# Optimization experiments

Hardware: AMD Instinct MI355X
Metric: run time of the kernel (lower is better)

The kernel has to match this reference:

```python
import jax, jax.numpy as jnp
import numpy as np

B, T, FD, NH, NC, NOUT = 32, 512, 256, 1024, 512, 8


def setup_inputs() -> dict:
    key = jax.random.key(0)
    ks = jax.random.split(key, 12)
    s = lambda k, sh, sc=0.05: (jax.random.normal(k, sh, jnp.float32) * sc)
    return dict(
        x=jax.random.normal(ks[0], (B, T, FD), jnp.float32),
        lens=jax.random.randint(ks[1], (B,), T // 2, T + 1, jnp.int32),
        W1=s(ks[2], (NH, FD)), b1=jnp.zeros((NH,), jnp.float32),
        g1=jnp.ones((NH,), jnp.float32), be1=jnp.zeros((NH,), jnp.float32),
        W2=s(ks[3], (NH, NH)), b2=jnp.zeros((NH,), jnp.float32),
        g2=jnp.ones((NH,), jnp.float32), be2=jnp.zeros((NH,), jnp.float32),
        lstm_wih=s(ks[4], (2, 2, 4 * NC, NH)),   # [layer, dir, 4H, in]
        lstm_whh=s(ks[5], (2, 2, 4 * NC, NC)),   # [layer, dir, 4H, H]
        lstm_bih=s(ks[6], (2, 2, 4 * NC)),
        lstm_bhh=s(ks[7], (2, 2, 4 * NC)),
        w_u=s(ks[8], (2 * NC,)), b_u=jnp.zeros((), jnp.float32),
        Wc=s(ks[9], (NOUT, 2 * NC)), bc=jnp.zeros((NOUT,), jnp.float32),
    )


def _layernorm(x, g, b, eps=1e-5):
    m = x.mean(-1, keepdims=True)
    v = ((x - m) ** 2).mean(-1, keepdims=True)
    return (x - m) / jnp.sqrt(v + eps) * g + b


def _lrelu(z):
    return jnp.where(z >= 0, z, 0.01 * z)  # LeakyReLU default slope


def _lstm_dir(x, wih, whh, bih, bhh):
    # x: [B,T,in] -> h: [B,T,H]; torch gate order i,f,g,o
    Bz = x.shape[0]
    H = whh.shape[1]
    xp = jnp.einsum('bti,gi->btg', x, wih) + bih + bhh  # [B,T,4H]

    def step(carry, xt):
        h, c = carry
        gates = xt + h @ whh.T
        i, f, g, o = jnp.split(gates, 4, axis=-1)
        c = jax.nn.sigmoid(f) * c + jax.nn.sigmoid(i) * jnp.tanh(g)
        h = jax.nn.sigmoid(o) * jnp.tanh(c)
        return (h, c), h

    h0 = jnp.zeros((Bz, H), x.dtype)
    _, hs = jax.lax.scan(step, (h0, h0), xp.transpose(1, 0, 2))
    return hs.transpose(1, 0, 2)


def _bilstm(x, wih, whh, bih, bhh):
    # params indexed [dir, ...]; backward dir processes the full padded
    # sequence reversed (original feeds unpacked pad_sequence to nn.LSTM)
    hf = _lstm_dir(x, wih[0], whh[0], bih[0], bhh[0])
    hb = _lstm_dir(x[:, ::-1], wih[1], whh[1], bih[1], bhh[1])[:, ::-1]
    return jnp.concatenate([hf, hb], axis=-1)


def reference(x, lens, W1, b1, g1, be1, W2, b2, g2, be2,
              lstm_wih, lstm_whh, lstm_bih, lstm_bhh, w_u, b_u, Wc, bc):
    Tn = x.shape[1]
    # extract MLP (dropout = identity in eval)
    h = _lrelu(_layernorm(x @ W1.T + b1, g1, be1))
    h = _lrelu(_layernorm(h @ W2.T + b2, g2, be2))
    # pad_sequence zero-pads AFTER extract -> zero out pad positions
    mask = jnp.arange(Tn)[None, :] < lens[:, None]  # [B,T]
    h = h * mask[..., None]
    # 2-layer bidirectional LSTM over the full padded sequence
    h = _bilstm(h, lstm_wih[0], lstm_whh[0], lstm_bih[0], lstm_bhh[0])
    h = _bilstm(h, lstm_wih[1], lstm_whh[1], lstm_bih[1], lstm_bhh[1])
    # Attn with window_len=1: per-step linear score, masked softmax, weighted sum
    scores = h @ w_u + b_u                          # [B,T]
    scores = jnp.where(mask, scores, -jnp.inf)
    alpha = jax.nn.softmax(scores, axis=-1)
    pooled = jnp.einsum('bt,btd->bd', alpha, h)     # [B, 2*NC]
    return pooled @ Wc.T + bc
```

## Files before the change

kernel.cpp:

```cpp
#include <hip/hip_runtime.h>
#include <stdint.h>
#include <stddef.h>


typedef short  short8  __attribute__((ext_vector_type(8)));
typedef short  short4v __attribute__((ext_vector_type(4)));
typedef float  float4v __attribute__((ext_vector_type(4)));
typedef unsigned long long u64;

__device__ inline float b2f(short x){
  union { unsigned u; float f; } v; v.u = ((unsigned)(unsigned short)x) << 16; return v.f;
}
__device__ inline short f2b(float f){
  union { float f; unsigned u; } v; v.f = f;
  unsigned r = (v.u + 0x7fffu + ((v.u >> 16) & 1u)) >> 16;
  return (short)r;
}
__device__ inline float sigm(float x){ return 1.f / (1.f + __expf(-x)); }
__device__ inline float tanh_(float x){ return 2.f / (1.f + __expf(-2.f*x)) - 1.f; }

__global__ __launch_bounds__(256) void detect_f32(
    const unsigned short* __restrict__ p, unsigned* __restrict__ flag)
{
  const int tid = threadIdx.x;
  unsigned h = 0;
  for (int i = tid; i < 1024; i += 256){
    const unsigned e = (p[i] >> 7) & 0xFFu;
    if (e >= 0xC0u) ++h;
  }
#pragma unroll
  for (int off=32; off>0; off>>=1) h += __shfl_xor(h, off, 64);
  __shared__ unsigned sh[4];
  if ((tid&63)==0) sh[tid>>6] = h;
  __syncthreads();
  if (tid==0) *flag = (sh[0]+sh[1]+sh[2]+sh[3] >= 8u) ? 1u : 0u;
}

__global__ __launch_bounds__(256) void to_bf16(
    const void* __restrict__ src, short* __restrict__ dst, int n,
    const unsigned* __restrict__ flag)
{
  const int i = blockIdx.x*256 + threadIdx.x;
  if (i >= n) return;
  if (*flag) dst[i] = f2b(((const float*)src)[i]);
  else       dst[i] = ((const short*)src)[i];
}

__global__ __launch_bounds__(256) void to_bf16_perm(
    const void* __restrict__ src, short* __restrict__ dst, const int W,
    const int n, const unsigned* __restrict__ flag)
{
  const int i = blockIdx.x*256 + threadIdx.x;
  if (i >= n) return;
  const int col = i % W;
  const int r   = (i / W) % 2048;
  const int blk = i / (W * 2048);
  const int gate = r >> 9, unit = r & 511;
  const size_t j = ((size_t)blk*2048 + (size_t)(unit*4 + gate))*W + col;
  short out = (*flag) ? f2b(((const float*)src)[i]) : ((const short*)src)[i];
  dst[j] = out;
}

__global__ __launch_bounds__(256) void gemm_bt(
    const short* __restrict__ A, const short* __restrict__ W,
    short* __restrict__ C, const short* __restrict__ bias1,
    const short* __restrict__ bias2, int N, int K)
{
  __shared__ __align__(16) short lA[128*40];
  __shared__ __align__(16) short lW[128*40];
  const int tid  = threadIdx.x;
  const int lane = tid & 63, wv = tid >> 6;
  const int wm = wv >> 1, wn = wv & 1;
  const int quad = lane >> 4, l15 = lane & 15;
  const long m0 = (long)blockIdx.y * 128, n0 = (long)blockIdx.x * 128;

  float4v acc[4][4];
#pragma unroll
  for (int i=0;i<4;++i)
#pragma unroll
    for (int j=0;j<4;++j) acc[i][j] = (float4v)0.f;

  const int r  = tid >> 2;
  const int kc = tid & 3;
  const int nkt = K >> 5;
  for (int kt = 0; kt < nkt; ++kt) {
    __syncthreads();
    const short* ga = A + (m0 + r) * (long)K + kt*32 + kc*8;
    const short* gw = W + (n0 + r) * (long)K + kt*32 + kc*8;
    short8 a0 = *(const short8*)ga;
    short8 a1 = *(const short8*)(ga + 64*(long)K);
    short8 w0 = *(const short8*)gw;
    short8 w1 = *(const short8*)(gw + 64*(long)K);
    *(short8*)&lA[r*40 + kc*8]        = a0;
    *(short8*)&lA[(r+64)*40 + kc*8]   = a1;
    *(short8*)&lW[r*40 + kc*8]        = w0;
    *(short8*)&lW[(r+64)*40 + kc*8]   = w1;
    __syncthreads();
    short8 af[4], bfr[4];
#pragma unroll
    for (int i=0;i<4;++i) af[i]  = *(const short8*)&lA[(wm*64 + i*16 + l15)*40 + quad*8];
#pragma unroll
    for (int j=0;j<4;++j) bfr[j] = *(const short8*)&lW[(wn*64 + j*16 + l15)*40 + quad*8];
#pragma unroll
    for (int i=0;i<4;++i)
#pragma unroll
      for (int j=0;j<4;++j)
        acc[i][j] = __builtin_amdgcn_mfma_f32_16x16x32_bf16(af[i], bfr[j], acc[i][j], 0, 0, 0);
  }
#pragma unroll
  for (int j=0;j<4;++j){
    const long n = n0 + wn*64 + j*16 + l15;
    float bs = b2f(bias1[n]);
    if (bias2) bs += b2f(bias2[n]);
#pragma unroll
    for (int i=0;i<4;++i){
      const long mb = m0 + wm*64 + i*16 + quad*4;
#pragma unroll
      for (int g=0; g<4; ++g)
        C[(mb+g)*(long)N + n] = f2b(acc[i][j][g] + bs);
    }
  }
}

__global__ __launch_bounds__(256) void ln_lrelu(
    const short* __restrict__ X, const short* __restrict__ g,
    const short* __restrict__ be, short* __restrict__ out,
    const int* __restrict__ lens, const int domask)
{
  const int row = blockIdx.x, tid = threadIdx.x;
  const short* xr = X + (size_t)row * 1024;
  short4v xv = *(const short4v*)(xr + tid*4);
  float v[4];
#pragma unroll
  for (int k=0;k<4;++k) v[k] = b2f(xv[k]);
  float s  = v[0]+v[1]+v[2]+v[3];
  float sq = v[0]*v[0]+v[1]*v[1]+v[2]*v[2]+v[3]*v[3];
#pragma unroll
  for (int off=32; off>0; off>>=1){
    s  += __shfl_xor(s,  off, 64);
    sq += __shfl_xor(sq, off, 64);
  }
  __shared__ float red[8];
  if ((tid&63)==0){ red[tid>>6] = s; red[4+(tid>>6)] = sq; }
  __syncthreads();
  s  = red[0]+red[1]+red[2]+red[3];
  sq = red[4]+red[5]+red[6]+red[7];
  const float mean = s * (1.f/1024.f);
  const float var  = sq * (1.f/1024.f) - mean*mean;
  const float rstd = rsqrtf(var + 1e-5f);
  float zmul = 1.f;
  if (domask){ const int b = row >> 9, t = row & 511; if (t >= lens[b]) zmul = 0.f; }
  short4v o;
#pragma unroll
  for (int k=0;k<4;++k){
    const int n = tid*4 + k;
    float y = (v[k]-mean)*rstd*b2f(g[n]) + b2f(be[n]);
    y = (y >= 0.f) ? y : 0.01f*y;
    o[k] = f2b(y * zmul);
  }
  *(short4v*)(out + (size_t)row*1024 + tid*4) = o;
}

__global__ __launch_bounds__(256) void lstm_scan(
    const short* __restrict__ xp, const int xp_cols, const int dir0,
    const short* __restrict__ whh,
    u64* __restrict__ hstate,
    short* __restrict__ hout,
    const unsigned epoch)
{
  const int wg = blockIdx.x;
  const int dloc = wg >> 5, d = dir0 + dloc;
  const int u0 = (wg & 31) * 16;
  const int tid = threadIdx.x, lane = tid & 63, wv = tid >> 6;
  const int quad = lane >> 4, l15 = lane & 15;

  short8 af[16];
  {
    const int prow = (u0 + wv*4)*4 + l15;
    const short* wr = whh + ((size_t)d*2048 + prow)*512 + quad*8;
#pragma unroll
    for (int ks=0; ks<16; ++ks) af[ks] = *(const short8*)(wr + ks*32);
  }

  float cstA = 0.f, cstB = 0.f;
  __shared__ __align__(16) unsigned hsh[2][32*260];
  const unsigned tbase = epoch << 10;
  const int pair = (u0 >> 1) + wv*2 + (quad >> 1);
  const int bst  = l15 + ((quad & 1) << 4);

  for (int step=0; step<512; ++step){
    const int t = d ? (511-step) : step;
    short4v x0, x1;
    {
      const size_t gb = (size_t)dloc*2048 + (size_t)(u0 + wv*4 + quad)*4;
      x0 = *(const short4v*)(xp + ((size_t)l15*512      + t)*xp_cols + gb);
      x1 = *(const short4v*)(xp + ((size_t)(l15+16)*512 + t)*xp_cols + gb);
    }
    unsigned* stg = &hsh[step&1][tid];
    if (step == 0){
#pragma unroll
      for (int k=0;k<32;++k) stg[k*260] = 0u;
    } else {
      const u64* hq = hstate + ((size_t)(d*2 + (step&1))<<13) + tid;
      const unsigned tgt = tbase + (unsigned)step;
      u64 v[32];
      for(;;){
        unsigned ok = 1u;
#pragma unroll
        for (int k=0;k<32;++k)
          v[k] = __hip_atomic_load(hq + (size_t)k*256,
                                   __ATOMIC_RELAXED, __HIP_MEMORY_SCOPE_AGENT);
#pragma unroll
        for (int k=0;k<32;++k) ok &= (unsigned)((unsigned)(v[k] >> 32) == tgt);
        if (ok) break;
        __builtin_amdgcn_s_sleep(1);
      }
#pragma unroll
      for (int k=0;k<32;++k) stg[k*260] = (unsigned)v[k];
    }
    __syncthreads();

    float4v a0e, a0o, a1e, a1o;
#pragma unroll
    for (int g=0; g<4; ++g){
      a0e[g] = b2f(x0[g]); a1e[g] = b2f(x1[g]);
      a0o[g] = 0.f;        a1o[g] = 0.f;
    }
    const short* hs = (const short*)&hsh[step&1][0];
#pragma unroll
    for (int kp=0; kp<8; ++kp){
      short8 b0e = *(const short8*)(hs + (size_t)l15*520      + (2*kp)*32   + quad*8);
      short8 b0o = *(const short8*)(hs + (size_t)l15*520      + (2*kp+1)*32 + quad*8);
      short8 b1e = *(const short8*)(hs + (size_t)(l15+16)*520 + (2*kp)*32   + quad*8);
      short8 b1o = *(const short8*)(hs + (size_t)(l15+16)*520 + (2*kp+1)*32 + quad*8);
      a0e = __builtin_amdgcn_mfma_f32_16x16x32_bf16(af[2*kp],   b0e, a0e, 0, 0, 0);
      a0o = __builtin_amdgcn_mfma_f32_16x16x32_bf16(af[2*kp+1], b0o, a0o, 0, 0, 0);
      a1e = __builtin_amdgcn_mfma_f32_16x16x32_bf16(af[2*kp],   b1e, a1e, 0, 0, 0);
      a1o = __builtin_amdgcn_mfma_f32_16x16x32_bf16(af[2*kp+1], b1o, a1o, 0, 0, 0);
    }

    const float gi0 = a0e[0]+a0o[0], gf0 = a0e[1]+a0o[1];
    const float gg0 = a0e[2]+a0o[2], go0 = a0e[3]+a0o[3];
    const float gi1 = a1e[0]+a1o[0], gf1 = a1e[1]+a1o[1];
    const float gg1 = a1e[2]+a1o[2], go1 = a1e[3]+a1o[3];
    cstA = sigm(gf0)*cstA + sigm(gi0)*tanh_(gg0);
    const float h0 = sigm(go0)*tanh_(cstA);
    cstB = sigm(gf1)*cstB + sigm(gi1)*tanh_(gg1);
    const float h1 = sigm(go1)*tanh_(cstB);

    const unsigned own = (unsigned)(unsigned short)f2b(h0)
                       | ((unsigned)(unsigned short)f2b(h1) << 16);
    const unsigned oth = __shfl_xor(own, 16, 64);
    const unsigned payload = (quad & 1)
        ? ((oth >> 16) | (own & 0xFFFF0000u))
        : ((own & 0xFFFFu) | (oth << 16));
    const u64 pkt = ((u64)(tbase + (unsigned)step + 1u) << 32) | (u64)payload;
    __hip_atomic_store(hstate + ((size_t)(d*2 + ((step+1)&1))<<13)
                         + (size_t)bst*256 + pair,
                       pkt, __ATOMIC_RELAXED, __HIP_MEMORY_SCOPE_AGENT);
    *(unsigned*)&hout[((size_t)bst*512 + t)*1024 + d*512 + 2*pair] = payload;
  }
}

__global__ __launch_bounds__(256) void attn_cls(
    const short* __restrict__ hseq, const short* __restrict__ wu,
    const short* __restrict__ Wc, const short* __restrict__ bc,
    const int* __restrict__ lens, float* __restrict__ out)
{
  const int b = blockIdx.x, tid = threadIdx.x, lane = tid & 63, wv = tid >> 6;
  const int len = lens[b];
  __shared__ float wus[1024];
  __shared__ float sc[512];
  __shared__ float redx[8];
  __shared__ float pooled[1024];
  for (int i=tid; i<1024; i+=256) wus[i] = b2f(wu[i]);
  __syncthreads();
  const short* hb = hseq + (size_t)b*512*1024;
  for (int t=wv; t<512; t+=4){
    const short* hr = hb + (size_t)t*1024;
    float s = 0.f;
#pragma unroll
    for (int j=0;j<16;++j) s += b2f(hr[lane + j*64]) * wus[lane + j*64];
#pragma unroll
    for (int off=32; off>0; off>>=1) s += __shfl_xor(s, off, 64);
    if (lane==0) sc[t] = (t < len) ? s : -3.0e38f;
  }
  __syncthreads();
  float m = -3.0e38f;
  for (int i=tid;i<512;i+=256) m = fmaxf(m, sc[i]);
#pragma unroll
  for (int off=32; off>0; off>>=1) m = fmaxf(m, __shfl_xor(m, off, 64));
  if (lane==0) redx[wv] = m;
  __syncthreads();
  m = fmaxf(fmaxf(redx[0],redx[1]), fmaxf(redx[2],redx[3]));
  float ssum = 0.f;
  for (int i=tid;i<512;i+=256){
    float e = (i<len) ? __expf(sc[i]-m) : 0.f;
    sc[i] = e;
    ssum += e;
  }
#pragma unroll
  for (int off=32; off>0; off>>=1) ssum += __shfl_xor(ssum, off, 64);
  if (lane==0) redx[4+wv] = ssum;
  __syncthreads();
  ssum = redx[4]+redx[5]+redx[6]+redx[7];
  const float inv = 1.f/ssum;
  float4v pa = (float4v)0.f;
  const int k0 = tid*4;
  for (int t=0; t<len; ++t){
    const float a = sc[t];
    short4v hv = *(const short4v*)(hb + (size_t)t*1024 + k0);
    pa[0] += a*b2f(hv[0]); pa[1] += a*b2f(hv[1]);
    pa[2] += a*b2f(hv[2]); pa[3] += a*b2f(hv[3]);
  }
  pooled[k0+0] = pa[0]*inv; pooled[k0+1] = pa[1]*inv;
  pooled[k0+2] = pa[2]*inv; pooled[k0+3] = pa[3]*inv;
  __syncthreads();
  const int j = tid >> 5, l32 = tid & 31;
  float s2 = 0.f;
  for (int kk=l32; kk<1024; kk+=32) s2 += b2f(Wc[j*1024+kk]) * pooled[kk];
#pragma unroll
  for (int off=16; off>0; off>>=1) s2 += __shfl_xor(s2, off, 32);
  if (l32==0) out[b*8+j] = s2 + b2f(bc[j]);
}

extern "C" void kernel_launch(void* const* d_in, const int* in_sizes, int n_in,
                              void* d_out, int out_size, void* d_ws, size_t ws_size,
                              hipStream_t stream)
{
  (void)in_sizes; (void)n_in; (void)out_size;
  const int*   lens = (const int*)d_in[1];
  float* outp = (float*)d_out;

  const size_t SZ_XP_A = (size_t)16384*4096*2;
  const size_t SZ_XP_B = (size_t)16384*2048*2;
  const size_t SZ_H    = (size_t)16384*1024*2;
  const size_t SZ_HS   = 262144;
  const size_t SZ_CNT  = 16384;
  const size_t SZ_NORM = 37000000;
  const bool planA = ws_size >= SZ_XP_A + 2*SZ_H + SZ_HS + SZ_CNT + SZ_NORM;
  const bool planB = !planA && ws_size >= SZ_XP_B + 2*SZ_H + SZ_HS + SZ_CNT + SZ_NORM;
  if (!planA && !planB) return;
  const size_t xpsz = planA ? SZ_XP_A : SZ_XP_B;

  char* ws = (char*)d_ws;
  short*    XP  = (short*)ws;
  short*    HB  = (short*)(ws + xpsz);
  short*    HC  = (short*)(ws + xpsz + SZ_H);
  u64*      HS64= (u64*)(ws + xpsz + 2*SZ_H);
  unsigned* CNT = (unsigned*)(ws + xpsz + 2*SZ_H + SZ_HS);
  unsigned* FLAG = CNT + 4000;
  short*    pool = (short*)(ws + xpsz + 2*SZ_H + SZ_HS + SZ_CNT);

  size_t off = 0;
  auto carve = [&](size_t n){ short* p = pool + off; off += (n + 127) & ~(size_t)127; return p; };
  short* x   = carve(4194304);
  short* W1  = carve(262144);
  short* b1  = carve(1024);
  short* g1  = carve(1024);
  short* be1 = carve(1024);
  short* W2  = carve(1048576);
  short* b2  = carve(1024);
  short* g2  = carve(1024);
  short* be2 = carve(1024);
  short* wih = carve(8388608);
  short* whh = carve(4194304);
  short* bih = carve(8192);
  short* bhh = carve(8192);
  short* wu  = carve(1024);
  short* Wc  = carve(8192);
  short* bc  = carve(8);

  hipMemsetAsync(HS64, 0, SZ_HS, stream);
  detect_f32<<<1, 256, 0, stream>>>((const unsigned short*)d_in[0], FLAG);

  struct { int idx; short* dst; int n; } cv[12] = {
    {0,x,4194304},{2,W1,262144},{3,b1,1024},{4,g1,1024},{5,be1,1024},
    {6,W2,1048576},{7,b2,1024},{8,g2,1024},{9,be2,1024},
    {14,wu,1024},{16,Wc,8192},{17,bc,8}
  };
  for (int i=0;i<12;++i)
    to_bf16<<<(cv[i].n + 255)/256, 256, 0, stream>>>(d_in[cv[i].idx], cv[i].dst, cv[i].n, FLAG);
  struct { int idx; short* dst; int W; int n; } pv[4] = {
    {10,wih,1024,8388608},{11,whh,512,4194304},{12,bih,1,8192},{13,bhh,1,8192}
  };
  for (int i=0;i<4;++i)
    to_bf16_perm<<<(pv[i].n + 255)/256, 256, 0, stream>>>(d_in[pv[i].idx], pv[i].dst,
                                                          pv[i].W, pv[i].n, FLAG);

  dim3 blk(256);
  gemm_bt<<<dim3(8,128),  blk, 0, stream>>>(x,  W1, XP, b1, nullptr, 1024, 256);
  ln_lrelu<<<16384, blk, 0, stream>>>(XP, g1, be1, HB, lens, 0);
  gemm_bt<<<dim3(8,128),  blk, 0, stream>>>(HB, W2, XP, b2, nullptr, 1024, 1024);
  ln_lrelu<<<16384, blk, 0, stream>>>(XP, g2, be2, HC, lens, 1);

  const short* lin[2]  = { HC, HB };
  short*       lout[2] = { HB, HC };
  for (int l = 0; l < 2; ++l){
    const short* whh_l = whh + (size_t)l*2*2048*512;
    if (planA){
      gemm_bt<<<dim3(32,128), blk, 0, stream>>>(
          lin[l], wih + (size_t)l*4096*1024, XP,
          bih + l*4096, bhh + l*4096, 4096, 1024);
      lstm_scan<<<64, blk, 0, stream>>>(XP, 4096, 0, whh_l, HS64, lout[l],
                                        (unsigned)(l+1));
    } else {
      for (int d = 0; d < 2; ++d){
        gemm_bt<<<dim3(16,128), blk, 0, stream>>>(
            lin[l], wih + ((size_t)(l*2+d))*2048*1024, XP,
            bih + (l*2+d)*2048, bhh + (l*2+d)*2048, 2048, 1024);
        lstm_scan<<<32, blk, 0, stream>>>(XP, 2048, d, whh_l, HS64, lout[l],
                                          (unsigned)(l+1));
      }
    }
  }
  attn_cls<<<32, blk, 0, stream>>>(HC, wu, Wc, bc, lens, outp);
}
```

Measured before the change: 4.350 ms.

## Prefetch next-step input projections, poll a single flag, and publish h early

The next timestep's input-projection loads are issued during the current step, after the cross-workgroup wait, so their global latency is hidden behind the MFMA work. The spin-wait now polls one packet word in a tight inner loop rather than reloading all 32 packets on every retry. The gate epilogue is split per batch half so the first half's hidden state is stored and published before the second half is computed, which may shorten the recurrent critical path. The cost is extra live registers and a slightly more complex control flow.

```diff
diff --git a/kernel.cpp b/kernel.cpp
--- a/kernel.cpp
+++ b/kernel.cpp
@@ -186,18 +186,26 @@
   __shared__ __align__(16) unsigned hsh[2][32*260];
   const unsigned tbase = epoch << 10;
   const int pair = (u0 >> 1) + wv*2 + (quad >> 1);
-  const int bst  = l15 + ((quad & 1) << 4);
+
+  const size_t gb = (size_t)dloc*2048 + (size_t)(u0 + wv*4 + quad)*4;
+  const short* xpA = xp + (size_t)l15*512*xp_cols + gb;
+  const short* xpB = xp + (size_t)(l15+16)*512*xp_cols + gb;
+
+  short4v xc0, xc1;
+  {
+    const int t0 = d ? 511 : 0;
+    xc0 = *(const short4v*)(xpA + (size_t)t0*xp_cols);
+    xc1 = *(const short4v*)(xpB + (size_t)t0*xp_cols);
+  }
 
   for (int step=0; step<512; ++step){
     const int t = d ? (511-step) : step;
-    short4v x0, x1;
-    {
-      const size_t gb = (size_t)dloc*2048 + (size_t)(u0 + wv*4 + quad)*4;
-      x0 = *(const short4v*)(xp + ((size_t)l15*512      + t)*xp_cols + gb);
-      x1 = *(const short4v*)(xp + ((size_t)(l15+16)*512 + t)*xp_cols + gb);
-    }
+    short4v xn0 = (short4v)0, xn1 = (short4v)0;
     unsigned* stg = &hsh[step&1][tid];
     if (step == 0){
+      const int tn = d ? 510 : 1;
+      xn0 = *(const short4v*)(xpA + (size_t)tn*xp_cols);
+      xn1 = *(const short4v*)(xpB + (size_t)tn*xp_cols);
 #pragma unroll
       for (int k=0;k<32;++k) stg[k*260] = 0u;
     } else {
@@ -213,8 +221,18 @@
 #pragma unroll
         for (int k=0;k<32;++k) ok &= (unsigned)((unsigned)(v[k] >> 32) == tgt);
         if (ok) break;
-        __builtin_amdgcn_s_sleep(1);
+        for(;;){
+          u64 s0 = __hip_atomic_load(hq, __ATOMIC_RELAXED,
+                                     __HIP_MEMORY_SCOPE_AGENT);
+          if ((unsigned)(s0 >> 32) == tgt) break;
+          __builtin_amdgcn_s_sleep(1);
+        }
       }
+      if (step < 511){
+        const int tn = d ? (510-step) : (step+1);
+        xn0 = *(const short4v*)(xpA + (size_t)tn*xp_cols);
+        xn1 = *(const short4v*)(xpB + (size_t)tn*xp_cols);
+      }
 #pragma unroll
       for (int k=0;k<32;++k) stg[k*260] = (unsigned)v[k];
     }
@@ -223,8 +241,8 @@
     float4v a0e, a0o, a1e, a1o;
 #pragma unroll
     for (int g=0; g<4; ++g){
-      a0e[g] = b2f(x0[g]); a1e[g] = b2f(x1[g]);
-      a0o[g] = 0.f;        a1o[g] = 0.f;
+      a0e[g] = b2f(xc0[g]); a1e[g] = b2f(xc1[g]);
+      a0o[g] = 0.f;         a1o[g] = 0.f;
     }
     const short* hs = (const short*)&hsh[step&1][0];
 #pragma unroll
@@ -239,26 +257,38 @@
       a1o = __builtin_amdgcn_mfma_f32_16x16x32_bf16(af[2*kp+1], b1o, a1o, 0, 0, 0);
     }
 
-    const float gi0 = a0e[0]+a0o[0], gf0 = a0e[1]+a0o[1];
-    const float gg0 = a0e[2]+a0o[2], go0 = a0e[3]+a0o[3];
-    const float gi1 = a1e[0]+a1o[0], gf1 = a1e[1]+a1o[1];
-    const float gg1 = a1e[2]+a1o[2], go1 = a1e[3]+a1o[3];
-    cstA = sigm(gf0)*cstA + sigm(gi0)*tanh_(gg0);
-    const float h0 = sigm(go0)*tanh_(cstA);
-    cstB = sigm(gf1)*cstB + sigm(gi1)*tanh_(gg1);
-    const float h1 = sigm(go1)*tanh_(cstB);
-
-    const unsigned own = (unsigned)(unsigned short)f2b(h0)
-                       | ((unsigned)(unsigned short)f2b(h1) << 16);
-    const unsigned oth = __shfl_xor(own, 16, 64);
-    const unsigned payload = (quad & 1)
-        ? ((oth >> 16) | (own & 0xFFFF0000u))
-        : ((own & 0xFFFFu) | (oth << 16));
-    const u64 pkt = ((u64)(tbase + (unsigned)step + 1u) << 32) | (u64)payload;
-    __hip_atomic_store(hstate + ((size_t)(d*2 + ((step+1)&1))<<13)
-                         + (size_t)bst*256 + pair,
-                       pkt, __ATOMIC_RELAXED, __HIP_MEMORY_SCOPE_AGENT);
-    *(unsigned*)&hout[((size_t)bst*512 + t)*1024 + d*512 + 2*pair] = payload;
+    u64* hdst = hstate + ((size_t)(d*2 + ((step+1)&1))<<13);
+    const u64 tag = (u64)(tbase + (unsigned)step + 1u) << 32;
+
+    {
+      const float gi = a0e[0]+a0o[0], gf = a0e[1]+a0o[1];
+      const float gg = a0e[2]+a0o[2], go = a0e[3]+a0o[3];
+      cstA = sigm(gf)*cstA + sigm(gi)*tanh_(gg);
+      const float h0 = sigm(go)*tanh_(cstA);
+      const unsigned h0u = (unsigned)(unsigned short)f2b(h0);
+      const unsigned o0  = __shfl_xor(h0u, 16, 64);
+      if ((quad & 1) == 0){
+        const unsigned pay = h0u | (o0 << 16);
+        __hip_atomic_store(hdst + (size_t)l15*256 + pair, tag | pay,
+                           __ATOMIC_RELAXED, __HIP_MEMORY_SCOPE_AGENT);
+        *(unsigned*)&hout[((size_t)l15*512 + t)*1024 + d*512 + 2*pair] = pay;
+      }
+    }
+    {
+      const float gi = a1e[0]+a1o[0], gf = a1e[1]+a1o[1];
+      const float gg = a1e[2]+a1o[2], go = a1e[3]+a1o[3];
+      cstB = sigm(gf)*cstB + sigm(gi)*tanh_(gg);
+      const float h1 = sigm(go)*tanh_(cstB);
+      const unsigned h1u = (unsigned)(unsigned short)f2b(h1);
+      const unsigned o1  = __shfl_xor(h1u, 16, 64);
+      if (quad & 1){
+        const unsigned pay = (o1 & 0xFFFFu) | (h1u << 16);
+        __hip_atomic_store(hdst + (size_t)(l15+16)*256 + pair, tag | pay,
+                           __ATOMIC_RELAXED, __HIP_MEMORY_SCOPE_AGENT);
+        *(unsigned*)&hout[((size_t)(l15+16)*512 + t)*1024 + d*512 + 2*pair] = pay;
+      }
+    }
+    xc0 = xn0; xc1 = xn1;
   }
 }
 
```

Result: slower. 4.552 ms (+4.6%).
